# Kernel tuning notes

Hardware: AMD Instinct MI355X
Metric: run time of the kernel (lower is better)

## Reference

```python
import jax, jax.numpy as jnp
import numpy as np

N_NODES = 50000
N_EDGES = 800000
N_GRAPHS = 64
IN_DIM = 128
HID = 128
S, C = 4, 16
DIM1 = 3 * S * S  # 48
OUT_DIM = DIM1 * C  # 768


def gcn_conv(x, W, b, src, dst, w):
    """PyG GCNConv: linear transform, then sym-normalized aggregation with self-loops (weight 1)."""
    n = x.shape[0]
    h = x @ W  # [N, out]
    deg = jnp.zeros((n,), x.dtype).at[dst].add(w) + 1.0  # self-loop weight 1
    dinv = jax.lax.rsqrt(deg)
    norm = dinv[src] * w * dinv[dst]  # [E]
    agg = jnp.zeros_like(h).at[dst].add(h[src] * norm[:, None])
    agg = agg + h * (1.0 / deg)[:, None]  # self-loop messages
    return agg + b


def setup_inputs() -> dict:
    key = jax.random.key(0)
    ks = jax.random.split(key, 16)
    x = jax.random.normal(ks[0], (N_NODES, IN_DIM), jnp.float32)
    edge_index = jax.random.randint(ks[1], (2, N_EDGES), 0, N_NODES, jnp.int64)
    edge_attr = jax.random.uniform(ks[2], (N_EDGES,), jnp.float32)
    batch = jnp.sort(jax.random.randint(ks[3], (N_NODES,), 0, N_GRAPHS, jnp.int64))

    def glorot(k, fan_in, fan_out):
        s = np.sqrt(6.0 / (fan_in + fan_out)).astype(np.float32)
        return jax.random.uniform(k, (fan_in, fan_out), jnp.float32, -s, s)

    return {
        "x": x, "edge_index": edge_index, "edge_attr": edge_attr, "batch": batch,
        "W1": glorot(ks[4], IN_DIM, HID), "b1": jnp.zeros((HID,), jnp.float32),
        "W2": glorot(ks[5], HID, HID // 2), "b2": jnp.zeros((HID // 2,), jnp.float32),
        "W3": glorot(ks[6], HID // 2, HID // 4), "b3": jnp.zeros((HID // 4,), jnp.float32),
        "Wl": glorot(ks[7], HID // 4, OUT_DIM), "bl": jnp.zeros((OUT_DIM,), jnp.float32),
    }


def reference(x, edge_index, edge_attr, batch, W1, b1, W2, b2, W3, b3, Wl, bl):
    src, dst = edge_index[0], edge_index[1]
    w = edge_attr / edge_attr.max()
    h = jax.nn.relu(gcn_conv(x, W1, b1, src, dst, w))
    h = jax.nn.relu(gcn_conv(h, W2, b2, src, dst, w))
    h = jax.nn.relu(gcn_conv(h, W3, b3, src, dst, w))
    # global mean pool over graphs
    sums = jax.ops.segment_sum(h, batch, num_segments=N_GRAPHS)
    cnt = jax.ops.segment_sum(jnp.ones((h.shape[0],), h.dtype), batch, num_segments=N_GRAPHS)
    pooled = sums / jnp.maximum(cnt, 1.0)[:, None]
    out = pooled @ Wl + bl  # [G, OUT_DIM]
    return out.reshape(N_GRAPHS, DIM1, C)
```

## Files before the change

kernel.cpp:

```cpp
#include <hip/hip_runtime.h>
#include <hip/hip_bf16.h>

#define NN 50000
#define NE 800000
#define NG 64
#define OUTD 768

#define G1B ((NN + 63) / 64)
#define MAXB 128
#define SSEG 32
#define TTL 4
#define ESEG (NE / SSEG)
#define NTL (NN / TTL)
#define HRB (SSEG * TTL)

__device__ __forceinline__ float bflo(unsigned int u) { return __uint_as_float(u << 16); }
__device__ __forceinline__ float bfhi(unsigned int u) { return __uint_as_float(u & 0xffff0000u); }
__device__ __forceinline__ unsigned short f2bf(float f) {
    unsigned int u = __float_as_uint(f);
    return (unsigned short)((u + 0x7fffu + ((u >> 16) & 1u)) >> 16);
}
__device__ __forceinline__ unsigned int pack2bf(float lo, float hi) {
    return (unsigned int)f2bf(lo) | ((unsigned int)f2bf(hi) << 16);
}

typedef __attribute__((ext_vector_type(8))) short bf16x8;
typedef __attribute__((ext_vector_type(4))) float f32x4;
union FragU { uint4 u4; bf16x8 v; };

template <int K, int N>
constexpr int mfma_lds_bytes() { return (K / 32) * (N / 16) * 1024; }

template <int K, int N, typename TX>
__device__ __forceinline__ void mfma_gemm_body(char* smem,
                                               const TX* __restrict__ X,
                                               const float* __restrict__ W,
                                               unsigned short* __restrict__ Y,
                                               int nRows, int bx) {
    constexpr int NCT = N / 16;
    constexpr int KS = K / 32;
    const int tid = threadIdx.x;

    for (int q = tid; q < KS * NCT * 64; q += 256) {
        int lane = q & 63;
        int fi = q >> 6;
        int ct = fi % NCT, kc = fi / NCT;
        int col = ct * 16 + (lane & 15);
        int kb = kc * 32 + ((lane >> 4) << 3);
        uint4 w;
        w.x = pack2bf(W[(size_t)(kb + 0) * N + col], W[(size_t)(kb + 1) * N + col]);
        w.y = pack2bf(W[(size_t)(kb + 2) * N + col], W[(size_t)(kb + 3) * N + col]);
        w.z = pack2bf(W[(size_t)(kb + 4) * N + col], W[(size_t)(kb + 5) * N + col]);
        w.w = pack2bf(W[(size_t)(kb + 6) * N + col], W[(size_t)(kb + 7) * N + col]);
        *(uint4*)(smem + (size_t)q * 16) = w;
    }
    __syncthreads();

    const int lane = tid & 63;
    const int wv = tid >> 6;
    const int m = lane & 15;
    const int quad = lane >> 4;
    const int row = bx * 64 + wv * 16 + m;
    const bool rowok = row < nRows;
    const TX* xr = X + (size_t)(rowok ? row : 0) * K;

    f32x4 acc[NCT];
#pragma unroll
    for (int ct = 0; ct < NCT; ++ct) acc[ct] = (f32x4){0.f, 0.f, 0.f, 0.f};

#pragma unroll
    for (int kc = 0; kc < KS; ++kc) {
        const int k0 = kc * 32 + quad * 8;
        FragU a;
        if constexpr (sizeof(TX) == 4) {
            float4 a0 = make_float4(0.f, 0.f, 0.f, 0.f), a1 = a0;
            if (rowok) {
                a0 = *(const float4*)(xr + k0);
                a1 = *(const float4*)(xr + k0 + 4);
            }
            a.u4 = make_uint4(pack2bf(a0.x, a0.y), pack2bf(a0.z, a0.w),
                              pack2bf(a1.x, a1.y), pack2bf(a1.z, a1.w));
        } else {
            a.u4 = rowok ? *(const uint4*)(xr + k0) : make_uint4(0, 0, 0, 0);
        }
#pragma unroll
        for (int ct = 0; ct < NCT; ++ct) {
            FragU b;
            b.u4 = *(const uint4*)(smem + ((size_t)(kc * NCT + ct) * 64 + lane) * 16);
            acc[ct] = __builtin_amdgcn_mfma_f32_16x16x32_bf16(a.v, b.v, acc[ct], 0, 0, 0);
        }
    }

    const int orowb = bx * 64 + wv * 16 + quad * 4;
#pragma unroll
    for (int ct = 0; ct < NCT; ++ct) {
        int col = ct * 16 + m;
#pragma unroll
        for (int r = 0; r < 4; ++r) {
            int orow = orowb + r;
            if (orow < nRows) Y[(size_t)orow * N + col] = f2bf(acc[ct][r]);
        }
    }
}

template <int K, int N, typename TX>
__global__ __launch_bounds__(256) void mfma_gemm_kernel(const TX* __restrict__ X,
                                                        const float* __restrict__ W,
                                                        unsigned short* __restrict__ Y,
                                                        int nRows) {
    extern __shared__ char smem[];
    mfma_gemm_body<K, N>(smem, X, W, Y, nRows, blockIdx.x);
}

__global__ __launch_bounds__(256) void fused1_kernel(const float* __restrict__ x,
                                                     const float* __restrict__ W1,
                                                     unsigned short* __restrict__ bufA,
                                                     const float* __restrict__ ea,
                                                     unsigned int* wmax,
                                                     const int* __restrict__ dst,
                                                     int* __restrict__ rank,
                                                     unsigned short* __restrict__ pcnt) {
    extern __shared__ char smem[];
    const int b = blockIdx.x;
    if (b < G1B) {
        mfma_gemm_body<128, 128>(smem, x, W1, bufA, NN, b);
    } else if (b < G1B + MAXB) {
        float* red = (float*)smem;
        const int bb = b - G1B;
        const float4* ea4 = (const float4*)ea;
        float m = 0.0f;
        for (int i = bb * 256 + threadIdx.x; i < NE / 4; i += MAXB * 256) {
            float4 v = ea4[i];
            m = fmaxf(fmaxf(m, fmaxf(v.x, v.y)), fmaxf(v.z, v.w));
        }
        red[threadIdx.x] = m;
        __syncthreads();
        for (int off = 128; off > 0; off >>= 1) {
            if (threadIdx.x < off)
                red[threadIdx.x] = fmaxf(red[threadIdx.x], red[threadIdx.x + off]);
            __syncthreads();
        }
        if (threadIdx.x == 0) atomicMax(wmax, __float_as_uint(red[0]));
    } else {
        const int b2 = b - G1B - MAXB;
        const int seg = b2 >> 2;
        const int tile = b2 & 3;
        unsigned int* lcnt = (unsigned int*)smem;
        for (int i = threadIdx.x; i < NTL / 2; i += 256) lcnt[i] = 0;
        __syncthreads();
        const int base = seg * ESEG;
        const int nlo = tile * NTL;
        const int4* dst4 = (const int4*)(dst + base);
        for (int g = threadIdx.x; g < ESEG / 4; g += 256) {
            const int4 v = dst4[g];
            const int e0 = base + g * 4;
            const int dd[4] = {v.x, v.y, v.z, v.w};
#pragma unroll
            for (int j = 0; j < 4; ++j) {
                int d = dd[j] - nlo;
                if ((unsigned)d < (unsigned)NTL) {
                    unsigned sh = (unsigned)(d & 1) << 4;
                    unsigned old = atomicAdd(&lcnt[d >> 1], 1u << sh);
                    rank[e0 + j] = (int)((old >> sh) & 0xffffu);
                }
            }
        }
        __syncthreads();
        unsigned int* prow32 = (unsigned int*)(pcnt + (size_t)seg * NN + nlo);
        for (int i = threadIdx.x; i < NTL / 2; i += 256) prow32[i] = lcnt[i];
    }
}

__global__ __launch_bounds__(256) void comb_kernel(unsigned short* __restrict__ pcnt,
                                                   int* __restrict__ hist,
                                                   int* __restrict__ blocksum) {
    __shared__ int red[256];
    int n = blockIdx.x * 256 + threadIdx.x;
    int run = 0;
    if (n < NN) {
#pragma unroll
        for (int s = 0; s < SSEG; ++s) {
            size_t idx = (size_t)s * NN + n;
            int v = pcnt[idx];
            pcnt[idx] = (unsigned short)run;
            run += v;
        }
        hist[n] = run;
    }
    red[threadIdx.x] = (n < NN) ? run : 0;
    __syncthreads();
    for (int off = 128; off > 0; off >>= 1) {
        if (threadIdx.x < off) red[threadIdx.x] += red[threadIdx.x + off];
        __syncthreads();
    }
    if (threadIdx.x == 0) blocksum[blockIdx.x] = red[0];
}

__global__ __launch_bounds__(256) void scan3_kernel(const int* __restrict__ hist,
                                                    const int* __restrict__ blocksum,
                                                    int* __restrict__ rowptr, int n, int nb) {
    __shared__ int sb[256];
    __shared__ int s[256];
    const int tid = threadIdx.x;
    int bv = (tid < nb) ? blocksum[tid] : 0;
    sb[tid] = bv;
    __syncthreads();
    for (int off = 1; off < 256; off <<= 1) {
        int t = (tid >= off) ? sb[tid - off] : 0;
        __syncthreads();
        sb[tid] += t;
        __syncthreads();
    }
    const int boff = (blockIdx.x > 0) ? sb[blockIdx.x - 1] : 0;
    const int total = sb[nb - 1];

    int i = blockIdx.x * 256 + tid;
    int v = (i < n) ? hist[i] : 0;
    s[tid] = v;
    __syncthreads();
    for (int off = 1; off < 256; off <<= 1) {
        int t = (tid >= off) ? s[tid - off] : 0;
        __syncthreads();
        s[tid] += t;
        __syncthreads();
    }
    if (i < n) rowptr[i] = boff + s[tid] - v;
    if (blockIdx.x == 0 && tid == 0) rowptr[n] = total;
}

__global__ void scat_kernel(const int* __restrict__ src, const int* __restrict__ dst,
                            const float* __restrict__ ea,
                            const int* __restrict__ rowptr,
                            const unsigned short* __restrict__ pcnt,
                            const int* __restrict__ rank,
                            int2* __restrict__ epack, int nE) {
    int e = blockIdx.x * blockDim.x + threadIdx.x;
    if (e >= nE) return;
    int s = e / ESEG;
    int d = dst[e];
    int pos = rowptr[d] + (int)pcnt[(size_t)s * NN + d] + rank[e];
    epack[pos] = make_int2(src[e], __float_as_int(ea[e]));
}

__global__ void deg_kernel(const int2* __restrict__ epack, const int* __restrict__ rowptr,
                           const unsigned int* __restrict__ wmax,
                           float* __restrict__ nrm, float* __restrict__ invdeg, int n) {
    int i = blockIdx.x * blockDim.x + threadIdx.x;
    if (i >= n) return;
    float rw = 1.0f / __uint_as_float(*wmax);
    float srw = sqrtf(rw);
    int s0 = rowptr[i], s1 = rowptr[i + 1];
    float s = 0.f;
    for (int e = s0; e < s1; ++e) s += __int_as_float(epack[e].y);
    float d = fmaf(s, rw, 1.0f);
    nrm[i] = rsqrtf(d) * srw;
    invdeg[i] = 1.0f / d;
}

template <int D>
__global__ __launch_bounds__(256) void agg_kernel(const unsigned short* __restrict__ H,
                                                  const int* __restrict__ rowptr,
                                                  const int2* __restrict__ epack,
                                                  const float* __restrict__ invdeg,
                                                  const float* __restrict__ nrm,
                                                  const float* __restrict__ bias,
                                                  unsigned short* __restrict__ out,
                                                  int nNodes) {
    constexpr int LPE = D / 8;
    constexpr int EPW = 64 / LPE;
    const int lane = threadIdx.x & 63;
    const int n = (blockIdx.x << 2) | (threadIdx.x >> 6);
    if (n >= nNodes) return;
    const int esub = lane / LPE;
    const int f8 = (lane % LPE) * 8;
    const int s0 = rowptr[n];
    const int cnt = rowptr[n + 1] - s0;
    const int2* ep = epack + s0;
    const float dn = nrm[n];

    float a[8] = {};
#define AGG8(c_, u_)                                                            \
    a[0] = fmaf(c_, bflo(u_.x), a[0]); a[1] = fmaf(c_, bfhi(u_.x), a[1]);       \
    a[2] = fmaf(c_, bflo(u_.y), a[2]); a[3] = fmaf(c_, bfhi(u_.y), a[3]);       \
    a[4] = fmaf(c_, bflo(u_.z), a[4]); a[5] = fmaf(c_, bfhi(u_.z), a[5]);       \
    a[6] = fmaf(c_, bflo(u_.w), a[6]); a[7] = fmaf(c_, bfhi(u_.w), a[7]);

    int kb = 0;
    for (; kb + 4 * EPW <= cnt; kb += 4 * EPW) {
        const int2 p0 = ep[kb + 0 * EPW + esub];
        const int2 p1 = ep[kb + 1 * EPW + esub];
        const int2 p2 = ep[kb + 2 * EPW + esub];
        const int2 p3 = ep[kb + 3 * EPW + esub];
        const uint4 u0 = *(const uint4*)(H + (size_t)p0.x * D + f8);
        const uint4 u1 = *(const uint4*)(H + (size_t)p1.x * D + f8);
        const uint4 u2 = *(const uint4*)(H + (size_t)p2.x * D + f8);
        const uint4 u3 = *(const uint4*)(H + (size_t)p3.x * D + f8);
        const float c0 = nrm[p0.x] * __int_as_float(p0.y) * dn;
        const float c1 = nrm[p1.x] * __int_as_float(p1.y) * dn;
        const float c2 = nrm[p2.x] * __int_as_float(p2.y) * dn;
        const float c3 = nrm[p3.x] * __int_as_float(p3.y) * dn;
        AGG8(c0, u0) AGG8(c1, u1) AGG8(c2, u2) AGG8(c3, u3)
    }
    for (; kb + 2 * EPW <= cnt; kb += 2 * EPW) {
        const int2 p0 = ep[kb + esub];
        const int2 p1 = ep[kb + EPW + esub];
        const uint4 u0 = *(const uint4*)(H + (size_t)p0.x * D + f8);
        const uint4 u1 = *(const uint4*)(H + (size_t)p1.x * D + f8);
        const float c0 = nrm[p0.x] * __int_as_float(p0.y) * dn;
        const float c1 = nrm[p1.x] * __int_as_float(p1.y) * dn;
        AGG8(c0, u0) AGG8(c1, u1)
    }
    for (; kb < cnt; kb += EPW) {
        const int idx = kb + esub;
        const bool ok = idx < cnt;
        const int2 p = ok ? ep[idx] : make_int2(n, 0);
        const uint4 u = *(const uint4*)(H + (size_t)p.x * D + f8);
        const float c = ok ? nrm[p.x] * __int_as_float(p.y) * dn : 0.f;
        AGG8(c, u)
    }
#undef AGG8
#pragma unroll
    for (int off = LPE; off < 64; off <<= 1) {
#pragma unroll
        for (int j = 0; j < 8; ++j) a[j] += __shfl_xor(a[j], off);
    }
    if (esub == 0) {
        const float id = invdeg[n];
        const uint4 un = *(const uint4*)(H + (size_t)n * D + f8);
        const float4 b0 = *(const float4*)(bias + f8);
        const float4 b1 = *(const float4*)(bias + f8 + 4);
        float o[8];
        o[0] = fmaxf(fmaf(id, bflo(un.x), a[0]) + b0.x, 0.f);
        o[1] = fmaxf(fmaf(id, bfhi(un.x), a[1]) + b0.y, 0.f);
        o[2] = fmaxf(fmaf(id, bflo(un.y), a[2]) + b0.z, 0.f);
        o[3] = fmaxf(fmaf(id, bfhi(un.y), a[3]) + b0.w, 0.f);
        o[4] = fmaxf(fmaf(id, bflo(un.z), a[4]) + b1.x, 0.f);
        o[5] = fmaxf(fmaf(id, bfhi(un.z), a[5]) + b1.y, 0.f);
        o[6] = fmaxf(fmaf(id, bflo(un.w), a[6]) + b1.z, 0.f);
        o[7] = fmaxf(fmaf(id, bfhi(un.w), a[7]) + b1.w, 0.f);
        uint4 w;
        w.x = pack2bf(o[0], o[1]);
        w.y = pack2bf(o[2], o[3]);
        w.z = pack2bf(o[4], o[5]);
        w.w = pack2bf(o[6], o[7]);
        *(uint4*)(out + (size_t)n * D + f8) = w;
    }
}

__global__ __launch_bounds__(1024) void poolfin_kernel(const unsigned short* __restrict__ h,
                                                       const int* __restrict__ batch,
                                                       const float* __restrict__ Wl,
                                                       const float* __restrict__ bl,
                                                       float* __restrict__ out, int n) {
    const int g = blockIdx.x;
    int lo = 0, hi = n;
    while (lo < hi) { int m = (lo + hi) >> 1; if (batch[m] < g) lo = m + 1; else hi = m; }
    const int start = lo;
    lo = start; hi = n;
    while (lo < hi) { int m = (lo + hi) >> 1; if (batch[m] < g + 1) lo = m + 1; else hi = m; }
    const int end = lo;

    __shared__ float part[1024];
    __shared__ float spool[32];
    const int f = threadIdx.x & 31;
    const int r = threadIdx.x >> 5;
    float acc = 0.f;
    for (int i = start + r; i < end; i += 32)
        acc += __uint_as_float((unsigned int)h[(size_t)i * 32 + f] << 16);
    part[threadIdx.x] = acc;
    __syncthreads();
    if (threadIdx.x < 32) {
        float s = 0.f;
#pragma unroll
        for (int q = 0; q < 32; ++q) s += part[q * 32 + f];
        float inv = 1.0f / fmaxf((float)(end - start), 1.0f);
        spool[f] = s * inv;
    }
    __syncthreads();
    if (threadIdx.x < OUTD) {
        const int o = threadIdx.x;
        float a2 = bl[o];
#pragma unroll
        for (int k = 0; k < 32; ++k)
            a2 = fmaf(spool[k], Wl[k * OUTD + o], a2);
        out[(size_t)g * OUTD + o] = a2;
    }
}

extern "C" void kernel_launch(void* const* d_in, const int* in_sizes, int n_in,
                              void* d_out, int out_size, void* d_ws, size_t ws_size,
                              hipStream_t stream) {
    const float* x = (const float*)d_in[0];
    const int* eidx = (const int*)d_in[1];
    const float* ea = (const float*)d_in[2];
    const int* batch = (const int*)d_in[3];
    const float* W1 = (const float*)d_in[4];
    const float* b1 = (const float*)d_in[5];
    const float* W2 = (const float*)d_in[6];
    const float* b2 = (const float*)d_in[7];
    const float* W3 = (const float*)d_in[8];
    const float* b3 = (const float*)d_in[9];
    const float* Wl = (const float*)d_in[10];
    const float* bl = (const float*)d_in[11];
    const int* src = eidx;
    const int* dst = eidx + NE;

    char* p = (char*)d_ws;
    auto take = [&](size_t bytes) {
        char* r = p;
        p += (bytes + 255) & ~(size_t)255;
        return r;
    };
    float* nrm = (float*)take(NN * 4);
    float* invdeg = (float*)take(NN * 4);
    int* hist = (int*)take(NN * 4);
    int* rowptr = (int*)take((NN + 1) * 4);
    int* blocksum = (int*)take(256 * 4);
    int2* epack = (int2*)take((size_t)NE * 8);
    unsigned int* wmax = (unsigned int*)take(4);
    unsigned short* bufA = (unsigned short*)take((size_t)NN * 128 * 2);
    unsigned short* bufB = (unsigned short*)take((size_t)NN * 128 * 2);
    int* rank = (int*)bufB;
    unsigned short* pcnt = (unsigned short*)((char*)bufB + (size_t)NE * 4 + 256);

    const int nblk = (NN + 255) / 256;
    const int eblk = (NE + 255) / 256;

    hipMemsetAsync(wmax, 0, 4, stream);

    constexpr int LDS1 = mfma_lds_bytes<128, 128>();
    static_assert(LDS1 >= NTL * 2, "HR branch LDS (packed u16 counters) must fit");
    fused1_kernel<<<G1B + MAXB + HRB, 256, LDS1, stream>>>(x, W1, bufA, ea, wmax,
                                                           dst, rank, pcnt);
    comb_kernel<<<nblk, 256, 0, stream>>>(pcnt, hist, blocksum);
    scan3_kernel<<<nblk, 256, 0, stream>>>(hist, blocksum, rowptr, NN, nblk);
    scat_kernel<<<eblk, 256, 0, stream>>>(src, dst, ea, rowptr, pcnt, rank, epack, NE);
    deg_kernel<<<nblk, 256, 0, stream>>>(epack, rowptr, wmax, nrm, invdeg, NN);

    agg_kernel<128><<<(NN + 3) / 4, 256, 0, stream>>>(bufA, rowptr, epack, invdeg, nrm, b1, bufB, NN);
    mfma_gemm_kernel<128, 64, unsigned short>
        <<<G1B, 256, mfma_lds_bytes<128, 64>(), stream>>>(bufB, W2, bufA, NN);
    agg_kernel<64><<<(NN + 3) / 4, 256, 0, stream>>>(bufA, rowptr, epack, invdeg, nrm, b2, bufB, NN);
    mfma_gemm_kernel<64, 32, unsigned short>
        <<<G1B, 256, mfma_lds_bytes<64, 32>(), stream>>>(bufB, W3, bufA, NN);
    agg_kernel<32><<<(NN + 3) / 4, 256, 0, stream>>>(bufA, rowptr, epack, invdeg, nrm, b3, bufB, NN);

    poolfin_kernel<<<NG, 1024, 0, stream>>>(bufB, batch, Wl, bl, (float*)d_out, NN);
}
```

Before: 252.3 us.

## Pack edge-rank counters as u8, fuse comb and scan via grid barrier

Doubles the number of edge segments and halves the node tiles in the CSR-build branch, packing four 8-bit counters per LDS word instead of two 16-bit ones. Merges the per-node segment-prefix kernel and the global scan kernel into one kernel that syncs blocks through a spin-wait on an atomic flag, dropping the hist buffer and one launch. Also splits the degree-sum loop into two accumulators. The spin barrier relies on all 196 blocks being co-resident, and 8-bit ranks overflow if a node gets more than 255 in-edges within one segment.

```diff
diff --git a/kernel.cpp b/kernel.cpp
--- a/kernel.cpp
+++ b/kernel.cpp
@@ -8,8 +8,8 @@
 
 #define G1B ((NN + 63) / 64)
 #define MAXB 128
-#define SSEG 32
-#define TTL 4
+#define SSEG 64
+#define TTL 2
 #define ESEG (NE / SSEG)
 #define NTL (NN / TTL)
 #define HRB (SSEG * TTL)
@@ -143,10 +143,10 @@
         if (threadIdx.x == 0) atomicMax(wmax, __float_as_uint(red[0]));
     } else {
         const int b2 = b - G1B - MAXB;
-        const int seg = b2 >> 2;
-        const int tile = b2 & 3;
+        const int seg = b2 >> 1;
+        const int tile = b2 & 1;
         unsigned int* lcnt = (unsigned int*)smem;
-        for (int i = threadIdx.x; i < NTL / 2; i += 256) lcnt[i] = 0;
+        for (int i = threadIdx.x; i < NTL / 4; i += 256) lcnt[i] = 0;
         __syncthreads();
         const int base = seg * ESEG;
         const int nlo = tile * NTL;
@@ -159,50 +159,60 @@
             for (int j = 0; j < 4; ++j) {
                 int d = dd[j] - nlo;
                 if ((unsigned)d < (unsigned)NTL) {
-                    unsigned sh = (unsigned)(d & 1) << 4;
-                    unsigned old = atomicAdd(&lcnt[d >> 1], 1u << sh);
-                    rank[e0 + j] = (int)((old >> sh) & 0xffffu);
+                    unsigned sh = (unsigned)(d & 3) << 3;
+                    unsigned old = atomicAdd(&lcnt[d >> 2], 1u << sh);
+                    rank[e0 + j] = (int)((old >> sh) & 0xffu);
                 }
             }
         }
         __syncthreads();
-        unsigned int* prow32 = (unsigned int*)(pcnt + (size_t)seg * NN + nlo);
-        for (int i = threadIdx.x; i < NTL / 2; i += 256) prow32[i] = lcnt[i];
-    }
-}
-
-__global__ __launch_bounds__(256) void comb_kernel(unsigned short* __restrict__ pcnt,
-                                                   int* __restrict__ hist,
-                                                   int* __restrict__ blocksum) {
-    __shared__ int red[256];
-    int n = blockIdx.x * 256 + threadIdx.x;
+        unsigned short* prow = pcnt + (size_t)seg * NN + nlo;
+        for (int i = threadIdx.x; i < NTL / 4; i += 256) {
+            unsigned int w = lcnt[i];
+            uint2 o;
+            o.x = (w & 0xffu) | ((w & 0xff00u) << 8);
+            o.y = ((w >> 16) & 0xffu) | ((w >> 8) & 0xff0000u);
+            *(uint2*)(prow + i * 4) = o;
+        }
+    }
+}
+
+__global__ __launch_bounds__(256) void combscan_kernel(unsigned short* __restrict__ pcnt,
+                                                       int* __restrict__ blocksum,
+                                                       int* __restrict__ rowptr,
+                                                       unsigned int* __restrict__ syncf) {
+    __shared__ int sc[256];
+    __shared__ int sb[256];
+    const int tid = threadIdx.x;
+    const int n = blockIdx.x * 256 + tid;
     int run = 0;
     if (n < NN) {
-#pragma unroll
+#pragma unroll 16
         for (int s = 0; s < SSEG; ++s) {
             size_t idx = (size_t)s * NN + n;
             int v = pcnt[idx];
             pcnt[idx] = (unsigned short)run;
             run += v;
         }
-        hist[n] = run;
-    }
-    red[threadIdx.x] = (n < NN) ? run : 0;
-    __syncthreads();
-    for (int off = 128; off > 0; off >>= 1) {
-        if (threadIdx.x < off) red[threadIdx.x] += red[threadIdx.x + off];
-        __syncthreads();
-    }
-    if (threadIdx.x == 0) blocksum[blockIdx.x] = red[0];
-}
-
-__global__ __launch_bounds__(256) void scan3_kernel(const int* __restrict__ hist,
-                                                    const int* __restrict__ blocksum,
-                                                    int* __restrict__ rowptr, int n, int nb) {
-    __shared__ int sb[256];
-    __shared__ int s[256];
-    const int tid = threadIdx.x;
-    int bv = (tid < nb) ? blocksum[tid] : 0;
+    }
+    sc[tid] = run;
+    __syncthreads();
+    for (int off = 1; off < 256; off <<= 1) {
+        int t = (tid >= off) ? sc[tid - off] : 0;
+        __syncthreads();
+        sc[tid] += t;
+        __syncthreads();
+    }
+    if (tid == 0) blocksum[blockIdx.x] = sc[255];
+    __threadfence();
+    __syncthreads();
+    if (tid == 0) {
+        atomicAdd(syncf, 1u);
+        while (atomicAdd(syncf, 0u) < (unsigned)gridDim.x) {}
+    }
+    __syncthreads();
+    __threadfence();
+    int bv = (tid < (int)gridDim.x) ? blocksum[tid] : 0;
     sb[tid] = bv;
     __syncthreads();
     for (int off = 1; off < 256; off <<= 1) {
@@ -212,20 +222,8 @@
         __syncthreads();
     }
     const int boff = (blockIdx.x > 0) ? sb[blockIdx.x - 1] : 0;
-    const int total = sb[nb - 1];
-
-    int i = blockIdx.x * 256 + tid;
-    int v = (i < n) ? hist[i] : 0;
-    s[tid] = v;
-    __syncthreads();
-    for (int off = 1; off < 256; off <<= 1) {
-        int t = (tid >= off) ? s[tid - off] : 0;
-        __syncthreads();
-        s[tid] += t;
-        __syncthreads();
-    }
-    if (i < n) rowptr[i] = boff + s[tid] - v;
-    if (blockIdx.x == 0 && tid == 0) rowptr[n] = total;
+    if (n < NN) rowptr[n] = boff + sc[tid] - run;
+    if (blockIdx.x == gridDim.x - 1 && tid == 0) rowptr[NN] = sb[gridDim.x - 1];
 }
 
 __global__ void scat_kernel(const int* __restrict__ src, const int* __restrict__ dst,
@@ -250,9 +248,14 @@
     float rw = 1.0f / __uint_as_float(*wmax);
     float srw = sqrtf(rw);
     int s0 = rowptr[i], s1 = rowptr[i + 1];
-    float s = 0.f;
-    for (int e = s0; e < s1; ++e) s += __int_as_float(epack[e].y);
-    float d = fmaf(s, rw, 1.0f);
+    float sa = 0.f, sb = 0.f;
+    int e = s0;
+    for (; e + 2 <= s1; e += 2) {
+        sa += __int_as_float(epack[e].y);
+        sb += __int_as_float(epack[e + 1].y);
+    }
+    if (e < s1) sa += __int_as_float(epack[e].y);
+    float d = fmaf(sa + sb, rw, 1.0f);
     nrm[i] = rsqrtf(d) * srw;
     invdeg[i] = 1.0f / d;
 }
@@ -413,11 +416,11 @@
     };
     float* nrm = (float*)take(NN * 4);
     float* invdeg = (float*)take(NN * 4);
-    int* hist = (int*)take(NN * 4);
     int* rowptr = (int*)take((NN + 1) * 4);
     int* blocksum = (int*)take(256 * 4);
     int2* epack = (int2*)take((size_t)NE * 8);
-    unsigned int* wmax = (unsigned int*)take(4);
+    unsigned int* wmax = (unsigned int*)take(8);
+    unsigned int* syncf = wmax + 1;
     unsigned short* bufA = (unsigned short*)take((size_t)NN * 128 * 2);
     unsigned short* bufB = (unsigned short*)take((size_t)NN * 128 * 2);
     int* rank = (int*)bufB;
@@ -426,14 +429,13 @@
     const int nblk = (NN + 255) / 256;
     const int eblk = (NE + 255) / 256;
 
-    hipMemsetAsync(wmax, 0, 4, stream);
+    hipMemsetAsync(wmax, 0, 8, stream);
 
     constexpr int LDS1 = mfma_lds_bytes<128, 128>();
-    static_assert(LDS1 >= NTL * 2, "HR branch LDS (packed u16 counters) must fit");
+    static_assert(LDS1 >= NTL, "HR branch LDS (packed u8 counters) must fit");
     fused1_kernel<<<G1B + MAXB + HRB, 256, LDS1, stream>>>(x, W1, bufA, ea, wmax,
                                                            dst, rank, pcnt);
-    comb_kernel<<<nblk, 256, 0, stream>>>(pcnt, hist, blocksum);
-    scan3_kernel<<<nblk, 256, 0, stream>>>(hist, blocksum, rowptr, NN, nblk);
+    combscan_kernel<<<nblk, 256, 0, stream>>>(pcnt, blocksum, rowptr, syncf);
     scat_kernel<<<eblk, 256, 0, stream>>>(src, dst, ea, rowptr, pcnt, rank, epack, NE);
     deg_kernel<<<nblk, 256, 0, stream>>>(epack, rowptr, wmax, nrm, invdeg, NN);
 
```

Measured after the change: 277.0 us. 1.1x slower.
